# Optimization experiments

Hardware: AMD Instinct MI355X
Metric: run time of the kernel (lower is better)

## Reference

```python
import jax, jax.numpy as jnp
import numpy as np

B, L, C = 256, 256, 128
HID, H = 128, 4
D = HID // H            # 32
NUM_LAYERS = 2
NEG_SLOPE = 0.2
LN_EPS = 1e-5


def setup_inputs() -> dict:
    key = jax.random.key(0)
    ks = jax.random.split(key, 16)
    E = 4096
    x = jax.random.normal(ks[0], (B, L, C), dtype=jnp.float32)
    edge_index = jax.random.randint(ks[1], (2, E), 0, C, dtype=jnp.int64)
    s_in = 1.0 / np.sqrt(L)
    s_h = 1.0 / np.sqrt(HID)
    return {
        "x": x,
        "edge_index": edge_index,
        "emb_W": jax.random.normal(ks[2], (L, HID), jnp.float32) * s_in,
        "emb_b": jnp.zeros((HID,), jnp.float32),
        "lin_l_W": jax.random.normal(ks[3], (NUM_LAYERS, HID, HID), jnp.float32) * s_h,
        "lin_l_b": jnp.zeros((NUM_LAYERS, HID), jnp.float32),
        "lin_r_W": jax.random.normal(ks[4], (NUM_LAYERS, HID, HID), jnp.float32) * s_h,
        "lin_r_b": jnp.zeros((NUM_LAYERS, HID), jnp.float32),
        "att": jax.random.normal(ks[5], (NUM_LAYERS, H, D), jnp.float32) * (1.0 / np.sqrt(D)),
        "gat_bias": jnp.zeros((NUM_LAYERS, HID), jnp.float32),
        "ln_gamma": jnp.ones((NUM_LAYERS, HID), jnp.float32),
        "ln_beta": jnp.zeros((NUM_LAYERS, HID), jnp.float32),
        "proj_W": jax.random.normal(ks[6], (HID, L), jnp.float32) * s_h,
        "proj_b": jnp.zeros((L,), jnp.float32),
    }


def _batch_edges(edge_index):
    # replicate single-graph edges per batch sample with node offsets, then add self loops
    E = edge_index.shape[1]
    off = jnp.repeat(jnp.arange(B, dtype=edge_index.dtype) * C, E)
    src = jnp.tile(edge_index[0], B) + off
    dst = jnp.tile(edge_index[1], B) + off
    loop = jnp.arange(B * C, dtype=edge_index.dtype)
    return jnp.concatenate([src, loop]), jnp.concatenate([dst, loop])


def _layer_norm(x, g, b):
    mu = jnp.mean(x, axis=-1, keepdims=True)
    var = jnp.mean(jnp.square(x - mu), axis=-1, keepdims=True)
    return (x - mu) * jax.lax.rsqrt(var + LN_EPS) * g + b


def _gatv2(x, src, dst, Wl, bl, Wr, br, a, bias):
    N = x.shape[0]
    xl = (x @ Wl + bl).reshape(N, H, D)   # source-side transform
    xr = (x @ Wr + br).reshape(N, H, D)   # target-side transform
    e = jax.nn.leaky_relu(xl[src] + xr[dst], NEG_SLOPE)   # (E', H, D)
    logits = jnp.einsum('ehd,hd->eh', e, a)               # (E', H)
    m = jax.ops.segment_max(logits, dst, num_segments=N)
    p = jnp.exp(logits - m[dst])
    s = jax.ops.segment_sum(p, dst, num_segments=N)
    alpha = p / (s[dst] + 1e-16)
    out = jax.ops.segment_sum(xl[src] * alpha[:, :, None], dst, num_segments=N)
    return out.reshape(N, HID) + bias, alpha


def reference(x, edge_index, emb_W, emb_b, lin_l_W, lin_l_b, lin_r_W, lin_r_b,
              att, gat_bias, ln_gamma, ln_beta, proj_W, proj_b):
    src, dst = _batch_edges(edge_index)
    # (B, L, C) -> nodes are channels: (B*C, L) -> embed to HID
    h = x.transpose(0, 2, 1).reshape(B * C, L) @ emb_W + emb_b
    alpha = None
    for i in range(NUM_LAYERS):
        new_h, alpha = _gatv2(h, src, dst, lin_l_W[i], lin_l_b[i],
                              lin_r_W[i], lin_r_b[i], att[i], gat_bias[i])
        new_h = jax.nn.elu(new_h)
        h = h + new_h
        h = _layer_norm(h, ln_gamma[i], ln_beta[i])
        # dropout: eval mode, identity
    # attention map (to_dense_adj semantics: adj[b, src%C, dst%C] = mean_h(alpha), then transpose)
    b_idx = src // C
    dense = jnp.zeros((B, C, C), x.dtype).at[b_idx, src % C, dst % C].add(alpha.mean(axis=-1))
    attn_map = dense.transpose(0, 2, 1)
    out = (h @ proj_W + proj_b).reshape(B, C, L).transpose(0, 2, 1)  # (B, L, C)
    return out, attn_map
```

## Files before the change

### kernel.cpp

```cpp
#include <hip/hip_runtime.h>
#include <hip/hip_fp16.h>
#include <math.h>

#define BB 256
#define LL 256
#define CC 128
#define HIDD 128
#define HH 4
#define DD 32
#define EE 4096
#define NN (BB*CC)
#define NEG_SLOPE 0.2f
#define LN_EPS 1e-5f
#define LOGCAP 59
#define DEGMAX 58
#define ASLOT 4352
#define AEDGE 4224

typedef short bf16x8 __attribute__((ext_vector_type(8)));
typedef float f32x4 __attribute__((ext_vector_type(4)));

__device__ __forceinline__ float red64(float p) {
    p += __shfl_xor(p, 32);
    p += __shfl_xor(p, 16);
    p += __shfl_xor(p, 8);
    p += __shfl_xor(p, 4);
    p += __shfl_xor(p, 2);
    p += __shfl_xor(p, 1);
    return p;
}
__device__ __forceinline__ unsigned bfr(float f) {
    unsigned x = __float_as_uint(f);
    return (x + 0x7FFFu + ((x >> 16) & 1u)) >> 16;
}
__device__ __forceinline__ unsigned pack2(float a, float b) { return bfr(a) | (bfr(b) << 16); }

__device__ __forceinline__ void stage_f32_rm(ushort* lds, const float* src, int ldm, int t) {
    #pragma unroll
    for (int i = 0; i < 8; ++i) {
        int flat = i*256 + t;
        int r = flat >> 4, c = flat & 15;
        const float* p = src + (size_t)r*ldm + c*8;
        float4 v0 = *(const float4*)p;
        float4 v1 = *(const float4*)(p + 4);
        uint4 pk;
        pk.x = pack2(v0.x, v0.y); pk.y = pack2(v0.z, v0.w);
        pk.z = pack2(v1.x, v1.y); pk.w = pack2(v1.z, v1.w);
        *(uint4*)&lds[((r*16) + (c ^ (r & 7)))*8] = pk;
    }
}
__device__ __forceinline__ void stage_bf16_rm(ushort* lds, const ushort* src, int ldm, int t) {
    #pragma unroll
    for (int i = 0; i < 8; ++i) {
        int flat = i*256 + t;
        int r = flat >> 4, c = flat & 15;
        uint4 pk = *(const uint4*)(src + (size_t)r*ldm + c*8);
        *(uint4*)&lds[((r*16) + (c ^ (r & 7)))*8] = pk;
    }
}
__device__ __forceinline__ void mfma_tile_128(const ushort* Als, const ushort* Bls,
                                              f32x4 acc[2][8], int w, int lane) {
    int mr = lane & 15, quad = lane >> 4;
    #pragma unroll
    for (int ks = 0; ks < 4; ++ks) {
        int ca = ks*4 + quad;
        bf16x8 a[2], b[8];
        #pragma unroll
        for (int mf = 0; mf < 2; ++mf) {
            int m = w*32 + mf*16 + mr;
            a[mf] = *(const bf16x8*)&Als[((m*16) + (ca ^ (m & 7)))*8];
        }
        #pragma unroll
        for (int nf = 0; nf < 8; ++nf) {
            int n = nf*16 + mr;
            b[nf] = *(const bf16x8*)&Bls[((n*16) + (ca ^ (n & 7)))*8];
        }
        #pragma unroll
        for (int mf = 0; mf < 2; ++mf)
            #pragma unroll
            for (int nf = 0; nf < 8; ++nf)
                acc[mf][nf] = __builtin_amdgcn_mfma_f32_16x16x32_bf16(a[mf], b[nf], acc[mf][nf], 0, 0, 0);
    }
}
#define ZERO_ACC(acc) { _Pragma("unroll") for (int i_=0;i_<2;++i_) { _Pragma("unroll") for (int j_=0;j_<8;++j_) acc[i_][j_] = (f32x4){0.f,0.f,0.f,0.f}; } }

__global__ __launch_bounds__(256) void prep_weights(const float* __restrict__ emb_W,
                                                    const float* __restrict__ lWl,
                                                    const float* __restrict__ lWr,
                                                    const float* __restrict__ pW,
                                                    ushort* __restrict__ WembT,
                                                    ushort* __restrict__ WlrT,
                                                    ushort* __restrict__ WpT) {
    int gid = blockIdx.x * 256 + threadIdx.x;
    float v[8];
    if (gid < 4096) {
        int f = gid >> 5, ch = gid & 31;
        #pragma unroll
        for (int j = 0; j < 8; ++j) v[j] = emb_W[(size_t)(ch*8 + j)*HIDD + f];
        uint4 pk; pk.x = pack2(v[0],v[1]); pk.y = pack2(v[2],v[3]);
        pk.z = pack2(v[4],v[5]); pk.w = pack2(v[6],v[7]);
        *(uint4*)&WembT[(size_t)f*LL + ch*8] = pk;
    } else if (gid < 12288) {
        int g = gid - 4096;
        int mat = g >> 11, f = (g >> 4) & 127, ch = g & 15;
        const float* src = ((mat & 1) ? lWr : lWl) + (size_t)(mat >> 1)*HIDD*HIDD;
        #pragma unroll
        for (int j = 0; j < 8; ++j) v[j] = src[(size_t)(ch*8 + j)*HIDD + f];
        uint4 pk; pk.x = pack2(v[0],v[1]); pk.y = pack2(v[2],v[3]);
        pk.z = pack2(v[4],v[5]); pk.w = pack2(v[6],v[7]);
        *(uint4*)&WlrT[(size_t)mat*HIDD*HIDD + (size_t)f*HIDD + ch*8] = pk;
    } else {
        int g = gid - 12288;
        int l = g >> 4, ch = g & 15;
        #pragma unroll
        for (int j = 0; j < 8; ++j) v[j] = pW[(size_t)(ch*8 + j)*LL + l];
        uint4 pk; pk.x = pack2(v[0],v[1]); pk.y = pack2(v[2],v[3]);
        pk.z = pack2(v[4],v[5]); pk.w = pack2(v[6],v[7]);
        *(uint4*)&WpT[(size_t)l*HIDD + ch*8] = pk;
    }
}

__global__ __launch_bounds__(256) void transpose_x(const float* __restrict__ x,
                                                   ushort* __restrict__ xbfT) {
    __shared__ float tile[CC][33];
    int b = blockIdx.y, l0 = blockIdx.x * 32;
    int t = threadIdx.x;
    #pragma unroll
    for (int i = 0; i < 4; ++i) {
        int flat = i*256 + t;
        int l = flat >> 5, c4 = flat & 31;
        float4 v = *(const float4*)&x[((size_t)b*LL + l0 + l)*CC + c4*4];
        tile[c4*4+0][l] = v.x; tile[c4*4+1][l] = v.y;
        tile[c4*4+2][l] = v.z; tile[c4*4+3][l] = v.w;
    }
    __syncthreads();
    #pragma unroll
    for (int i = 0; i < 2; ++i) {
        int flat = i*256 + t;
        int c = flat >> 2, ch = flat & 3;
        const float* p = &tile[c][ch*8];
        uint4 pk; pk.x = pack2(p[0],p[1]); pk.y = pack2(p[2],p[3]);
        pk.z = pack2(p[4],p[5]); pk.w = pack2(p[6],p[7]);
        *(uint4*)&xbfT[((size_t)b*CC + c)*LL + l0 + ch*8] = pk;
    }
}

__global__ __launch_bounds__(256) void build_csr(const int* __restrict__ edge,
                                                 int* __restrict__ csr_off,
                                                 int* __restrict__ csr_src) {
    __shared__ int cnt[CC];
    __shared__ int offs[CC+1];
    __shared__ int cur[CC];
    int t = threadIdx.x;
    if (t < CC) cnt[t] = 0;
    __syncthreads();
    for (int j = t; j < EE; j += 256) atomicAdd(&cnt[edge[EE + j]], 1);
    __syncthreads();
    if (t == 0) {
        int a = 0;
        for (int i = 0; i < CC; ++i) { offs[i] = a; a += cnt[i]; }
        offs[CC] = a;
    }
    __syncthreads();
    if (t < CC) cur[t] = offs[t];
    if (t <= CC) csr_off[t] = offs[t];
    __syncthreads();
    for (int j = t; j < EE; j += 256) {
        int pos = atomicAdd(&cur[edge[EE + j]], 1);
        csr_src[pos] = edge[j];
    }
}

__global__ __launch_bounds__(256) void embed_mfma(const ushort* __restrict__ xbfT,
                                                  const ushort* __restrict__ WembT,
                                                  const float* __restrict__ bias,
                                                  float* __restrict__ hout) {
    __shared__ __align__(16) ushort Als[128*16*8];
    __shared__ __align__(16) ushort Bls[128*16*8];
    int b = blockIdx.x;
    int t = threadIdx.x, lane = t & 63, w = t >> 6;
    f32x4 acc[2][8];
    ZERO_ACC(acc)
    #pragma unroll
    for (int kh = 0; kh < 2; ++kh) {
        if (kh) __syncthreads();
        stage_bf16_rm(Als, xbfT + (size_t)b*CC*LL + kh*128, LL, t);
        stage_bf16_rm(Bls, WembT + kh*128, LL, t);
        __syncthreads();
        mfma_tile_128(Als, Bls, acc, w, lane);
    }
    int mr = lane & 15, quad = lane >> 4;
    #pragma unroll
    for (int nf = 0; nf < 8; ++nf) {
        int f = nf*16 + mr;
        float bv = bias[f];
        #pragma unroll
        for (int mf = 0; mf < 2; ++mf)
            #pragma unroll
            for (int r = 0; r < 4; ++r) {
                int node = w*32 + mf*16 + quad*4 + r;
                hout[((size_t)b*CC + node)*HIDD + f] = acc[mf][nf][r] + bv;
            }
    }
}

__global__ __launch_bounds__(256) void lin_mfma(const float* __restrict__ hmat,
                                                const ushort* __restrict__ WlT,
                                                const ushort* __restrict__ WrT,
                                                const float* __restrict__ bl,
                                                const float* __restrict__ br,
                                                float* __restrict__ xlT,
                                                float* __restrict__ xrT) {
    __shared__ __align__(16) ushort Als[128*16*8];
    __shared__ __align__(16) ushort Bls[128*16*8];
    const ushort* W   = blockIdx.y ? WrT : WlT;
    const float* bias = blockIdx.y ? br : bl;
    float* out        = blockIdx.y ? xrT : xlT;
    int m0 = blockIdx.x * 128;
    int t = threadIdx.x, lane = t & 63, w = t >> 6;
    f32x4 acc[2][8];
    ZERO_ACC(acc)
    stage_f32_rm(Als, hmat + (size_t)m0*HIDD, HIDD, t);
    stage_bf16_rm(Bls, W, HIDD, t);
    __syncthreads();
    mfma_tile_128(Als, Bls, acc, w, lane);
    int mr = lane & 15, quad = lane >> 4;
    #pragma unroll
    for (int nf = 0; nf < 8; ++nf) {
        int f = nf*16 + mr;
        float bv = bias[f];
        int h = f >> 5, d = f & 31;
        #pragma unroll
        for (int mf = 0; mf < 2; ++mf)
            #pragma unroll
            for (int r = 0; r < 4; ++r) {
                int node = w*32 + mf*16 + quad*4 + r;
                out[(((size_t)blockIdx.x*HH + h)*CC + node)*DD + d] = acc[mf][nf][r] + bv;
            }
    }
}

__global__ __launch_bounds__(128) void gat_attn(const float* __restrict__ xlT,
                                                const float* __restrict__ xrT,
                                                const int* __restrict__ csr_off,
                                                const int* __restrict__ csr_src,
                                                const float* __restrict__ att,
                                                float* __restrict__ xagg,
                                                float* __restrict__ alpha_ws) {
    __shared__ unsigned xl2u[16*129];
    __shared__ __half logit_s[128*LOGCAP];
    __shared__ unsigned char csr_s[EE];
    int bid = blockIdx.x;
    int b = bid >> 2, h = bid & 3;
    int t = threadIdx.x;

    const float* xl_g = xlT + ((size_t)b*HH + h)*CC*DD;
    #pragma unroll
    for (int i = 0; i < 8; ++i) {
        int flat = i*128 + t;
        int n = flat >> 3, c = flat & 7;
        float4 v = *(const float4*)&xl_g[(size_t)n*DD + c*4];
        xl2u[(2*c+0)*129 + n] = pack2(v.x, v.y);
        xl2u[(2*c+1)*129 + n] = pack2(v.z, v.w);
    }
    #pragma unroll
    for (int i = 0; i < EE/128; ++i)
        csr_s[i*128 + t] = (unsigned char)csr_src[i*128 + t];

    float att_r[32], xr_r[32];
    const float* xr_g = xrT + (((size_t)b*HH + h)*CC + t) * DD;
    #pragma unroll
    for (int c = 0; c < 8; ++c) {
        float4 v = *(const float4*)&xr_g[c*4];
        xr_r[c*4+0]=v.x; xr_r[c*4+1]=v.y; xr_r[c*4+2]=v.z; xr_r[c*4+3]=v.w;
        float4 a = *(const float4*)&att[h*DD + c*4];
        att_r[c*4+0]=a.x; att_r[c*4+1]=a.y; att_r[c*4+2]=a.z; att_r[c*4+3]=a.w;
    }
    int base = csr_off[t];
    int deg  = csr_off[t+1] - base;
    if (deg > DEGMAX) deg = DEGMAX;
    __syncthreads();

    float m = -1e30f, s = 0.f;
    __half* mylog = &logit_s[t*LOGCAP];
    for (int j = 0; j <= deg; ++j) {
        int src = (j < deg) ? (int)csr_s[base + j] : t;
        float p0=0.f, p1=0.f, p2=0.f, p3=0.f;
        #pragma unroll
        for (int q = 0; q < 16; ++q) {
            unsigned u = xl2u[q*129 + src];
            float va = __uint_as_float(u << 16);
            float vb = __uint_as_float(u & 0xFFFF0000u);
            float w0 = va + xr_r[2*q];   w0 = fmaxf(w0, NEG_SLOPE*w0);
            float w1 = vb + xr_r[2*q+1]; w1 = fmaxf(w1, NEG_SLOPE*w1);
            if (q & 1) { p2 = fmaf(w0, att_r[2*q], p2); p3 = fmaf(w1, att_r[2*q+1], p3); }
            else       { p0 = fmaf(w0, att_r[2*q], p0); p1 = fmaf(w1, att_r[2*q+1], p1); }
        }
        float l = (p0+p1) + (p2+p3);
        mylog[j] = __float2half(l);
        float mn = fmaxf(m, l);
        s = s * __expf(m - mn) + __expf(l - mn);
        m = mn;
    }
    float is = 1.f / (s + 1e-16f);

    float acc_r[32];
    #pragma unroll
    for (int d = 0; d < 32; ++d) acc_r[d] = 0.f;
    for (int j = 0; j <= deg; ++j) {
        int src = (j < deg) ? (int)csr_s[base + j] : t;
        float alpha = __expf(__half2float(mylog[j]) - m) * is;
        if (alpha_ws) {
            int slot = (j < deg) ? (base + j) : (AEDGE + t);
            alpha_ws[(size_t)(b*HH + h)*ASLOT + slot] = alpha;
        }
        #pragma unroll
        for (int q = 0; q < 16; ++q) {
            unsigned u = xl2u[q*129 + src];
            acc_r[2*q+0] = fmaf(alpha, __uint_as_float(u << 16),         acc_r[2*q+0]);
            acc_r[2*q+1] = fmaf(alpha, __uint_as_float(u & 0xFFFF0000u), acc_r[2*q+1]);
        }
    }
    float* og = xagg + (((size_t)b*CC + t)*HH + h) * DD;
    #pragma unroll
    for (int c = 0; c < 8; ++c) {
        float4 o = make_float4(acc_r[c*4+0], acc_r[c*4+1], acc_r[c*4+2], acc_r[c*4+3]);
        *(float4*)&og[c*4] = o;
    }
}

__global__ __launch_bounds__(128) void gat_epilogue(const float* __restrict__ xagg,
                                                    const float* __restrict__ gbias,
                                                    const float* __restrict__ ln_g,
                                                    const float* __restrict__ ln_b,
                                                    const int* __restrict__ csr_off,
                                                    const int* __restrict__ csr_src,
                                                    const float* __restrict__ alpha_ws,
                                                    float* __restrict__ hmat,
                                                    float* __restrict__ attn_out) {
    __shared__ float attnrow[CC];
    __shared__ float wred[2], wred2[2];
    int node = blockIdx.x;
    int b = node >> 7, dstc = node & 127;
    int f = threadIdx.x;
    attnrow[f] = 0.f;

    float o = xagg[(size_t)node*HIDD + f] + gbias[f];
    o = o > 0.f ? o : (__expf(o) - 1.f);
    float hv = hmat[(size_t)node*HIDD + f] + o;

    float sum = red64(hv);
    if ((f & 63) == 0) wred[f >> 6] = sum;
    __syncthreads();
    float mean = (wred[0] + wred[1]) * 0.0078125f;
    float d = hv - mean;
    float q = red64(d * d);
    if ((f & 63) == 0) wred2[f >> 6] = q;
    __syncthreads();
    float var = (wred2[0] + wred2[1]) * 0.0078125f;
    hmat[(size_t)node*HIDD + f] = d * rsqrtf(var + LN_EPS) * ln_g[f] + ln_b[f];

    if (attn_out) {
        int base = csr_off[dstc];
        int deg  = csr_off[dstc+1] - base;
        if (deg > DEGMAX) deg = DEGMAX;
        for (int j = f; j < deg; j += 128) {
            float a = 0.f;
            #pragma unroll
            for (int hh = 0; hh < HH; ++hh)
                a += alpha_ws[(size_t)(b*HH + hh)*ASLOT + base + j];
            atomicAdd(&attnrow[csr_src[base + j]], 0.25f * a);
        }
        if (f == 0) {
            float a = 0.f;
            #pragma unroll
            for (int hh = 0; hh < HH; ++hh)
                a += alpha_ws[(size_t)(b*HH + hh)*ASLOT + AEDGE + dstc];
            atomicAdd(&attnrow[dstc], 0.25f * a);
        }
        __syncthreads();
        attn_out[(size_t)node*CC + f] = attnrow[f];
    }
}

__global__ __launch_bounds__(256) void proj_mfma(const float* __restrict__ hmat,
                                                 const ushort* __restrict__ WpT,
                                                 const float* __restrict__ bias,
                                                 float* __restrict__ out) {
    __shared__ __align__(16) ushort Als[128*16*8];
    __shared__ __align__(16) ushort Bls[128*16*8];
    int l0 = blockIdx.x * 128;
    int b  = blockIdx.y;
    int t = threadIdx.x, lane = t & 63, w = t >> 6;
    f32x4 acc[2][8];
    ZERO_ACC(acc)
    stage_bf16_rm(Als, WpT + (size_t)l0*HIDD, HIDD, t);
    stage_f32_rm(Bls, hmat + (size_t)b*CC*HIDD, HIDD, t);
    __syncthreads();
    mfma_tile_128(Als, Bls, acc, w, lane);
    int mr = lane & 15, quad = lane >> 4;
    #pragma unroll
    for (int nf = 0; nf < 8; ++nf) {
        int c = nf*16 + mr;
        #pragma unroll
        for (int mf = 0; mf < 2; ++mf)
            #pragma unroll
            for (int r = 0; r < 4; ++r) {
                int l = l0 + w*32 + mf*16 + quad*4 + r;
                out[((size_t)b*LL + l)*CC + c] = acc[mf][nf][r] + bias[l];
            }
    }
}

extern "C" void kernel_launch(void* const* d_in, const int* in_sizes, int n_in,
                              void* d_out, int out_size, void* d_ws, size_t ws_size,
                              hipStream_t stream) {
    const float* x        = (const float*)d_in[0];
    const int*   edge     = (const int*)d_in[1];
    const float* emb_W    = (const float*)d_in[2];
    const float* emb_b    = (const float*)d_in[3];
    const float* lin_l_W  = (const float*)d_in[4];
    const float* lin_l_b  = (const float*)d_in[5];
    const float* lin_r_W  = (const float*)d_in[6];
    const float* lin_r_b  = (const float*)d_in[7];
    const float* att      = (const float*)d_in[8];
    const float* gat_bias = (const float*)d_in[9];
    const float* ln_g     = (const float*)d_in[10];
    const float* ln_b     = (const float*)d_in[11];
    const float* proj_W   = (const float*)d_in[12];
    const float* proj_b   = (const float*)d_in[13];

    float* h     = (float*)d_ws;
    float* xlT   = h    + (size_t)NN * HIDD;
    float* xrT   = xlT  + (size_t)NN * HIDD;
    float* xagg  = xrT  + (size_t)NN * HIDD;
    float* shared_region = xagg + (size_t)NN * HIDD;
    float*  alpha = shared_region;
    ushort* xbfT  = (ushort*)shared_region;
    ushort* WembT = (ushort*)(shared_region + (size_t)BB*HH*ASLOT);
    ushort* WlrT  = WembT + (size_t)CC*LL;
    ushort* WpT   = WlrT + (size_t)4*HIDD*HIDD;
    int* csr_off  = (int*)(WpT + (size_t)LL*HIDD);
    int* csr_src  = csr_off + 132;

    float* out0 = (float*)d_out;
    float* attn = out0 + (size_t)BB * LL * CC;

    build_csr<<<1, 256, 0, stream>>>(edge, csr_off, csr_src);
    prep_weights<<<64, 256, 0, stream>>>(emb_W, lin_l_W, lin_r_W, proj_W, WembT, WlrT, WpT);
    transpose_x<<<dim3(8, BB), 256, 0, stream>>>(x, xbfT);
    embed_mfma<<<BB, 256, 0, stream>>>(xbfT, WembT, emb_b, h);
    for (int layer = 0; layer < 2; ++layer) {
        float* aws = (layer == 1) ? alpha : nullptr;
        lin_mfma<<<dim3(NN/128, 2), 256, 0, stream>>>(h,
            WlrT + (size_t)(layer*2 + 0)*HIDD*HIDD,
            WlrT + (size_t)(layer*2 + 1)*HIDD*HIDD,
            lin_l_b + layer*HIDD, lin_r_b + layer*HIDD,
            xlT, xrT);
        gat_attn<<<BB*HH, 128, 0, stream>>>(xlT, xrT, csr_off, csr_src,
            att + layer*HIDD, xagg, aws);
        gat_epilogue<<<NN, 128, 0, stream>>>(xagg,
            gat_bias + layer*HIDD, ln_g + layer*HIDD, ln_b + layer*HIDD,
            csr_off, csr_src, aws, h, (layer == 1) ? attn : nullptr);
    }
    proj_mfma<<<dim3(2, BB), 256, 0, stream>>>(h, WpT, proj_b, out0);
}
```

Baseline: 330.8 us.

## Compute GAT aggregation as dense bf16 MFMA matmul and simplify leaky-relu logit math

The attention kernel now scatters per-edge alpha into a per-block dense 128x128 bf16 adjacency in LDS. It then computes the weighted aggregation as a dense A·XL matrix multiply with MFMA instructions, replacing the per-thread scalar gather-FMA loop. The logit computation is rewritten algebraically: leaky_relu(z)*a becomes 0.6*p + 0.4*sign(a)*|p| with p = a*xl + a*xr precomputed. xl is stored as uint2 for wider LDS reads. Trade-offs: the dense matmul does extra work on the zeros, LDS use rises, and duplicate edges are summed in bf16, which adds rounding.

```diff
diff --git a/kernel.cpp b/kernel.cpp
--- a/kernel.cpp
+++ b/kernel.cpp
@@ -34,6 +34,8 @@
     return (x + 0x7FFFu + ((x >> 16) & 1u)) >> 16;
 }
 __device__ __forceinline__ unsigned pack2(float a, float b) { return bfr(a) | (bfr(b) << 16); }
+__device__ __forceinline__ float blo(unsigned u) { return __uint_as_float(u << 16); }
+__device__ __forceinline__ float bhi(unsigned u) { return __uint_as_float(u & 0xFFFF0000u); }
 
 __device__ __forceinline__ void stage_f32_rm(ushort* lds, const float* src, int ldm, int t) {
     #pragma unroll
@@ -247,8 +249,9 @@
                                                 const float* __restrict__ att,
                                                 float* __restrict__ xagg,
                                                 float* __restrict__ alpha_ws) {
-    __shared__ unsigned xl2u[16*129];
-    __shared__ __half logit_s[128*LOGCAP];
+    __shared__ __align__(16) uint2 xl4[8*129];
+    __shared__ __align__(16) ushort Adense[128][136];
+    __shared__ __align__(16) ushort scratch[7552];
     __shared__ unsigned char csr_s[EE];
     int bid = blockIdx.x;
     int b = bid >> 2, h = bid & 3;
@@ -260,43 +263,50 @@
         int flat = i*128 + t;
         int n = flat >> 3, c = flat & 7;
         float4 v = *(const float4*)&xl_g[(size_t)n*DD + c*4];
-        xl2u[(2*c+0)*129 + n] = pack2(v.x, v.y);
-        xl2u[(2*c+1)*129 + n] = pack2(v.z, v.w);
+        xl4[c*129 + n] = make_uint2(pack2(v.x, v.y), pack2(v.z, v.w));
     }
     #pragma unroll
     for (int i = 0; i < EE/128; ++i)
         csr_s[i*128 + t] = (unsigned char)csr_src[i*128 + t];
-
-    float att_r[32], xr_r[32];
+    #pragma unroll
+    for (int i = 0; i < 17; ++i)
+        *(uint4*)&Adense[t][i*8] = make_uint4(0,0,0,0);
+
+    float att_r[32], r_r[32], k1_r[32];
     const float* xr_g = xrT + (((size_t)b*HH + h)*CC + t) * DD;
     #pragma unroll
     for (int c = 0; c < 8; ++c) {
-        float4 v = *(const float4*)&xr_g[c*4];
-        xr_r[c*4+0]=v.x; xr_r[c*4+1]=v.y; xr_r[c*4+2]=v.z; xr_r[c*4+3]=v.w;
-        float4 a = *(const float4*)&att[h*DD + c*4];
-        att_r[c*4+0]=a.x; att_r[c*4+1]=a.y; att_r[c*4+2]=a.z; att_r[c*4+3]=a.w;
+        float4 xv = *(const float4*)&xr_g[c*4];
+        float4 av = *(const float4*)&att[h*DD + c*4];
+        att_r[c*4+0]=av.x; att_r[c*4+1]=av.y; att_r[c*4+2]=av.z; att_r[c*4+3]=av.w;
+        r_r[c*4+0]=av.x*xv.x; r_r[c*4+1]=av.y*xv.y; r_r[c*4+2]=av.z*xv.z; r_r[c*4+3]=av.w*xv.w;
+        k1_r[c*4+0]=copysignf(0.4f,av.x); k1_r[c*4+1]=copysignf(0.4f,av.y);
+        k1_r[c*4+2]=copysignf(0.4f,av.z); k1_r[c*4+3]=copysignf(0.4f,av.w);
     }
     int base = csr_off[t];
     int deg  = csr_off[t+1] - base;
     if (deg > DEGMAX) deg = DEGMAX;
     __syncthreads();
 
+    __half* mylog = (__half*)scratch + t*LOGCAP;
     float m = -1e30f, s = 0.f;
-    __half* mylog = &logit_s[t*LOGCAP];
     for (int j = 0; j <= deg; ++j) {
         int src = (j < deg) ? (int)csr_s[base + j] : t;
-        float p0=0.f, p1=0.f, p2=0.f, p3=0.f;
-        #pragma unroll
-        for (int q = 0; q < 16; ++q) {
-            unsigned u = xl2u[q*129 + src];
-            float va = __uint_as_float(u << 16);
-            float vb = __uint_as_float(u & 0xFFFF0000u);
-            float w0 = va + xr_r[2*q];   w0 = fmaxf(w0, NEG_SLOPE*w0);
-            float w1 = vb + xr_r[2*q+1]; w1 = fmaxf(w1, NEG_SLOPE*w1);
-            if (q & 1) { p2 = fmaf(w0, att_r[2*q], p2); p3 = fmaf(w1, att_r[2*q+1], p3); }
-            else       { p0 = fmaf(w0, att_r[2*q], p0); p1 = fmaf(w1, att_r[2*q+1], p1); }
+        float a0=0.f, a1=0.f, a2=0.f, a3=0.f;
+        #pragma unroll
+        for (int q = 0; q < 8; ++q) {
+            uint2 u = xl4[q*129 + src];
+            float p;
+            p = fmaf(att_r[4*q+0], blo(u.x), r_r[4*q+0]);
+            a0 = fmaf(0.6f, p, a0); a0 = fmaf(k1_r[4*q+0], fabsf(p), a0);
+            p = fmaf(att_r[4*q+1], bhi(u.x), r_r[4*q+1]);
+            a1 = fmaf(0.6f, p, a1); a1 = fmaf(k1_r[4*q+1], fabsf(p), a1);
+            p = fmaf(att_r[4*q+2], blo(u.y), r_r[4*q+2]);
+            a2 = fmaf(0.6f, p, a2); a2 = fmaf(k1_r[4*q+2], fabsf(p), a2);
+            p = fmaf(att_r[4*q+3], bhi(u.y), r_r[4*q+3]);
+            a3 = fmaf(0.6f, p, a3); a3 = fmaf(k1_r[4*q+3], fabsf(p), a3);
         }
-        float l = (p0+p1) + (p2+p3);
+        float l = (a0+a1) + (a2+a3);
         mylog[j] = __float2half(l);
         float mn = fmaxf(m, l);
         s = s * __expf(m - mn) + __expf(l - mn);
@@ -304,29 +314,57 @@
     }
     float is = 1.f / (s + 1e-16f);
 
-    float acc_r[32];
-    #pragma unroll
-    for (int d = 0; d < 32; ++d) acc_r[d] = 0.f;
+    float* aws = alpha_ws ? alpha_ws + (size_t)(b*HH + h)*ASLOT : nullptr;
     for (int j = 0; j <= deg; ++j) {
         int src = (j < deg) ? (int)csr_s[base + j] : t;
         float alpha = __expf(__half2float(mylog[j]) - m) * is;
-        if (alpha_ws) {
-            int slot = (j < deg) ? (base + j) : (AEDGE + t);
-            alpha_ws[(size_t)(b*HH + h)*ASLOT + slot] = alpha;
+        if (aws) aws[(j < deg) ? (base + j) : (AEDGE + t)] = alpha;
+        float cur = blo((unsigned)Adense[t][src]) + alpha;
+        Adense[t][src] = (ushort)bfr(cur);
+    }
+    __syncthreads();
+
+    ushort (*XLB)[136] = (ushort(*)[136])scratch;
+    #pragma unroll
+    for (int q = 0; q < 8; ++q) {
+        uint2 u = xl4[q*129 + t];
+        XLB[4*q+0][t] = (ushort)(u.x & 0xFFFFu);
+        XLB[4*q+1][t] = (ushort)(u.x >> 16);
+        XLB[4*q+2][t] = (ushort)(u.y & 0xFFFFu);
+        XLB[4*q+3][t] = (ushort)(u.y >> 16);
+    }
+    __syncthreads();
+
+    int lane = t & 63, w = t >> 6, mr = lane & 15, quad = lane >> 4;
+    f32x4 acc[4][2];
+    #pragma unroll
+    for (int mf = 0; mf < 4; ++mf)
+        #pragma unroll
+        for (int nf = 0; nf < 2; ++nf) acc[mf][nf] = (f32x4){0.f,0.f,0.f,0.f};
+    #pragma unroll
+    for (int ks = 0; ks < 4; ++ks) {
+        bf16x8 bB[2];
+        #pragma unroll
+        for (int nf = 0; nf < 2; ++nf)
+            bB[nf] = *(const bf16x8*)&XLB[nf*16 + mr][ks*32 + quad*8];
+        #pragma unroll
+        for (int mf = 0; mf < 4; ++mf) {
+            bf16x8 aA = *(const bf16x8*)&Adense[w*64 + mf*16 + mr][ks*32 + quad*8];
+            #pragma unroll
+            for (int nf = 0; nf < 2; ++nf)
+                acc[mf][nf] = __builtin_amdgcn_mfma_f32_16x16x32_bf16(aA, bB[nf], acc[mf][nf], 0, 0, 0);
         }
-        #pragma unroll
-        for (int q = 0; q < 16; ++q) {
-            unsigned u = xl2u[q*129 + src];
-            acc_r[2*q+0] = fmaf(alpha, __uint_as_float(u << 16),         acc_r[2*q+0]);
-            acc_r[2*q+1] = fmaf(alpha, __uint_as_float(u & 0xFFFF0000u), acc_r[2*q+1]);
-        }
-    }
-    float* og = xagg + (((size_t)b*CC + t)*HH + h) * DD;
-    #pragma unroll
-    for (int c = 0; c < 8; ++c) {
-        float4 o = make_float4(acc_r[c*4+0], acc_r[c*4+1], acc_r[c*4+2], acc_r[c*4+3]);
-        *(float4*)&og[c*4] = o;
-    }
+    }
+    #pragma unroll
+    for (int mf = 0; mf < 4; ++mf)
+        #pragma unroll
+        for (int nf = 0; nf < 2; ++nf)
+            #pragma unroll
+            for (int r = 0; r < 4; ++r) {
+                int dst = w*64 + mf*16 + quad*4 + r;
+                int d = nf*16 + mr;
+                xagg[(((size_t)b*CC + dst)*HH + h)*DD + d] = acc[mf][nf][r];
+            }
 }
 
 __global__ __launch_bounds__(128) void gat_epilogue(const float* __restrict__ xagg,
```

Measured after the change: 336.7 us. Within noise of the previous version (+1.8%).

## Split GAT attention edges across thread pairs and algebraically simplify leaky-relu logits

Applied to the files above, without the earlier changes.

Doubles the attention grid so each destination node is handled by two threads that process alternating edges, then combines max, sum and aggregation results with cross-lane shuffles. Leaky-relu times att is rewritten as 0.6*p + 0.4*sign(a)*|p| with p precomputed as a*(xl+xr), which removes the max operation per element. Only the CSR slice for the block's half of the destinations is staged, and xl is stored as uint2 for wider LDS reads. The intent is more parallelism and shorter serial edge loops, at the cost of restaging xl twice per (b,h) and extra shuffles. The rewritten logit form only matches the original when the linear part equals a*(xl+xr), which holds here.

```diff
diff --git a/kernel.cpp b/kernel.cpp
--- a/kernel.cpp
+++ b/kernel.cpp
@@ -12,8 +12,9 @@
 #define NN (BB*CC)
 #define NEG_SLOPE 0.2f
 #define LN_EPS 1e-5f
-#define LOGCAP 59
 #define DEGMAX 58
+#define LOG2CAP 31
+#define CSRSL 3840
 #define ASLOT 4352
 #define AEDGE 4224
 
@@ -34,6 +35,8 @@
     return (x + 0x7FFFu + ((x >> 16) & 1u)) >> 16;
 }
 __device__ __forceinline__ unsigned pack2(float a, float b) { return bfr(a) | (bfr(b) << 16); }
+__device__ __forceinline__ float blo(unsigned u) { return __uint_as_float(u << 16); }
+__device__ __forceinline__ float bhi(unsigned u) { return __uint_as_float(u & 0xFFFF0000u); }
 
 __device__ __forceinline__ void stage_f32_rm(ushort* lds, const float* src, int ldm, int t) {
     #pragma unroll
@@ -247,12 +250,13 @@
                                                 const float* __restrict__ att,
                                                 float* __restrict__ xagg,
                                                 float* __restrict__ alpha_ws) {
-    __shared__ unsigned xl2u[16*129];
-    __shared__ __half logit_s[128*LOGCAP];
-    __shared__ unsigned char csr_s[EE];
+    __shared__ __align__(16) uint2 xl4[8*129];
+    __shared__ __half mylog[128*LOG2CAP];
+    __shared__ unsigned char csr_s[CSRSL];
     int bid = blockIdx.x;
-    int b = bid >> 2, h = bid & 3;
+    int b = bid >> 3, h = (bid >> 1) & 3, half = bid & 1;
     int t = threadIdx.x;
+    int dst = half*64 + (t >> 1), p = t & 1;
 
     const float* xl_g = xlT + ((size_t)b*HH + h)*CC*DD;
     #pragma unroll
@@ -260,71 +264,92 @@
         int flat = i*128 + t;
         int n = flat >> 3, c = flat & 7;
         float4 v = *(const float4*)&xl_g[(size_t)n*DD + c*4];
-        xl2u[(2*c+0)*129 + n] = pack2(v.x, v.y);
-        xl2u[(2*c+1)*129 + n] = pack2(v.z, v.w);
-    }
-    #pragma unroll
-    for (int i = 0; i < EE/128; ++i)
-        csr_s[i*128 + t] = (unsigned char)csr_src[i*128 + t];
-
-    float att_r[32], xr_r[32];
-    const float* xr_g = xrT + (((size_t)b*HH + h)*CC + t) * DD;
+        xl4[c*129 + n] = make_uint2(pack2(v.x, v.y), pack2(v.z, v.w));
+    }
+    int rbase = csr_off[half*64];
+    int rcnt  = csr_off[half*64 + 64] - rbase;
+    if (rcnt > CSRSL) rcnt = CSRSL;
+    for (int j = t; j < rcnt; j += 128)
+        csr_s[j] = (unsigned char)csr_src[rbase + j];
+
+    float att_r[32], r_r[32], q_r[32];
+    const float* xr_g = xrT + (((size_t)b*HH + h)*CC + dst) * DD;
     #pragma unroll
     for (int c = 0; c < 8; ++c) {
-        float4 v = *(const float4*)&xr_g[c*4];
-        xr_r[c*4+0]=v.x; xr_r[c*4+1]=v.y; xr_r[c*4+2]=v.z; xr_r[c*4+3]=v.w;
-        float4 a = *(const float4*)&att[h*DD + c*4];
-        att_r[c*4+0]=a.x; att_r[c*4+1]=a.y; att_r[c*4+2]=a.z; att_r[c*4+3]=a.w;
-    }
-    int base = csr_off[t];
-    int deg  = csr_off[t+1] - base;
+        float4 xv = *(const float4*)&xr_g[c*4];
+        float4 av = *(const float4*)&att[h*DD + c*4];
+        att_r[c*4+0]=av.x; att_r[c*4+1]=av.y; att_r[c*4+2]=av.z; att_r[c*4+3]=av.w;
+        r_r[c*4+0]=av.x*xv.x; r_r[c*4+1]=av.y*xv.y; r_r[c*4+2]=av.z*xv.z; r_r[c*4+3]=av.w*xv.w;
+        q_r[c*4+0]=copysignf(0.4f,av.x); q_r[c*4+1]=copysignf(0.4f,av.y);
+        q_r[c*4+2]=copysignf(0.4f,av.z); q_r[c*4+3]=copysignf(0.4f,av.w);
+    }
+    int base = csr_off[dst];
+    int deg  = csr_off[dst+1] - base;
     if (deg > DEGMAX) deg = DEGMAX;
-    __syncthreads();
-
-    float m = -1e30f, s = 0.f;
-    __half* mylog = &logit_s[t*LOGCAP];
-    for (int j = 0; j <= deg; ++j) {
-        int src = (j < deg) ? (int)csr_s[base + j] : t;
-        float p0=0.f, p1=0.f, p2=0.f, p3=0.f;
-        #pragma unroll
-        for (int q = 0; q < 16; ++q) {
-            unsigned u = xl2u[q*129 + src];
-            float va = __uint_as_float(u << 16);
-            float vb = __uint_as_float(u & 0xFFFF0000u);
-            float w0 = va + xr_r[2*q];   w0 = fmaxf(w0, NEG_SLOPE*w0);
-            float w1 = vb + xr_r[2*q+1]; w1 = fmaxf(w1, NEG_SLOPE*w1);
-            if (q & 1) { p2 = fmaf(w0, att_r[2*q], p2); p3 = fmaf(w1, att_r[2*q+1], p3); }
-            else       { p0 = fmaf(w0, att_r[2*q], p0); p1 = fmaf(w1, att_r[2*q+1], p1); }
-        }
-        float l = (p0+p1) + (p2+p3);
-        mylog[j] = __float2half(l);
-        float mn = fmaxf(m, l);
-        s = s * __expf(m - mn) + __expf(l - mn);
-        m = mn;
-    }
+    int sbase = base - rbase;
+    __syncthreads();
+
+    __half* ml = &mylog[t*LOG2CAP];
+    float m = -1e30f;
+    int nv = 0;
+    for (int vj = p; vj <= deg; vj += 2, ++nv) {
+        int src = (vj < deg) ? (int)csr_s[sbase + vj] : dst;
+        float a0=0.f, a1=0.f, a2=0.f, a3=0.f;
+        #pragma unroll
+        for (int q = 0; q < 8; ++q) {
+            uint2 u = xl4[q*129 + src];
+            float pp;
+            pp = fmaf(att_r[4*q+0], blo(u.x), r_r[4*q+0]);
+            a0 = fmaf(0.6f, pp, a0); a0 = fmaf(q_r[4*q+0], fabsf(pp), a0);
+            pp = fmaf(att_r[4*q+1], bhi(u.x), r_r[4*q+1]);
+            a1 = fmaf(0.6f, pp, a1); a1 = fmaf(q_r[4*q+1], fabsf(pp), a1);
+            pp = fmaf(att_r[4*q+2], blo(u.y), r_r[4*q+2]);
+            a2 = fmaf(0.6f, pp, a2); a2 = fmaf(q_r[4*q+2], fabsf(pp), a2);
+            pp = fmaf(att_r[4*q+3], bhi(u.y), r_r[4*q+3]);
+            a3 = fmaf(0.6f, pp, a3); a3 = fmaf(q_r[4*q+3], fabsf(pp), a3);
+        }
+        float l = (a0+a1) + (a2+a3);
+        ml[nv] = __float2half(l);
+        m = fmaxf(m, l);
+    }
+    m = fmaxf(m, __shfl_xor(m, 1));
+
+    float s = 0.f;
+    for (int k = 0; k < nv; ++k) {
+        float e = __expf(__half2float(ml[k]) - m);
+        s += e;
+        ml[k] = __float2half(e);
+    }
+    s += __shfl_xor(s, 1);
     float is = 1.f / (s + 1e-16f);
 
     float acc_r[32];
     #pragma unroll
     for (int d = 0; d < 32; ++d) acc_r[d] = 0.f;
-    for (int j = 0; j <= deg; ++j) {
-        int src = (j < deg) ? (int)csr_s[base + j] : t;
-        float alpha = __expf(__half2float(mylog[j]) - m) * is;
-        if (alpha_ws) {
-            int slot = (j < deg) ? (base + j) : (AEDGE + t);
-            alpha_ws[(size_t)(b*HH + h)*ASLOT + slot] = alpha;
-        }
-        #pragma unroll
-        for (int q = 0; q < 16; ++q) {
-            unsigned u = xl2u[q*129 + src];
-            acc_r[2*q+0] = fmaf(alpha, __uint_as_float(u << 16),         acc_r[2*q+0]);
-            acc_r[2*q+1] = fmaf(alpha, __uint_as_float(u & 0xFFFF0000u), acc_r[2*q+1]);
-        }
-    }
-    float* og = xagg + (((size_t)b*CC + t)*HH + h) * DD;
-    #pragma unroll
-    for (int c = 0; c < 8; ++c) {
-        float4 o = make_float4(acc_r[c*4+0], acc_r[c*4+1], acc_r[c*4+2], acc_r[c*4+3]);
+    float* aws = alpha_ws ? alpha_ws + (size_t)(b*HH + h)*ASLOT : nullptr;
+    {
+        int vj = p;
+        for (int k = 0; k < nv; ++k, vj += 2) {
+            int src = (vj < deg) ? (int)csr_s[sbase + vj] : dst;
+            float alpha = __half2float(ml[k]) * is;
+            if (aws) aws[(vj < deg) ? (base + vj) : (AEDGE + dst)] = alpha;
+            #pragma unroll
+            for (int q = 0; q < 8; ++q) {
+                uint2 u = xl4[q*129 + src];
+                acc_r[4*q+0] = fmaf(alpha, blo(u.x), acc_r[4*q+0]);
+                acc_r[4*q+1] = fmaf(alpha, bhi(u.x), acc_r[4*q+1]);
+                acc_r[4*q+2] = fmaf(alpha, blo(u.y), acc_r[4*q+2]);
+                acc_r[4*q+3] = fmaf(alpha, bhi(u.y), acc_r[4*q+3]);
+            }
+        }
+    }
+    #pragma unroll
+    for (int d = 0; d < 32; ++d) acc_r[d] += __shfl_xor(acc_r[d], 1);
+    float* og = xagg + (((size_t)b*CC + dst)*HH + h) * DD + p*16;
+    #pragma unroll
+    for (int c = 0; c < 4; ++c) {
+        float4 o = make_float4(acc_r[p*16+c*4+0], acc_r[p*16+c*4+1],
+                               acc_r[p*16+c*4+2], acc_r[p*16+c*4+3]);
         *(float4*)&og[c*4] = o;
     }
 }
@@ -457,7 +482,7 @@
             WlrT + (size_t)(layer*2 + 1)*HIDD*HIDD,
             lin_l_b + layer*HIDD, lin_r_b + layer*HIDD,
             xlT, xrT);
-        gat_attn<<<BB*HH, 128, 0, stream>>>(xlT, xrT, csr_off, csr_src,
+        gat_attn<<<BB*HH*2, 128, 0, stream>>>(xlT, xrT, csr_off, csr_src,
             att + layer*HIDD, xagg, aws);
         gat_epilogue<<<NN, 128, 0, stream>>>(xagg,
             gat_bias + layer*HIDD, ln_g + layer*HIDD, ln_b + layer*HIDD,
```

Result: faster. 313.9 us (-5.1%).
